# Kernel tuning notes

Hardware: AMD Instinct MI355X
Metric: run time of the kernel (lower is better)

The kernel has to match this reference:

```python
import jax, jax.numpy as jnp
import numpy as np

NUM_GROUPS = 32
NUM_HEAD_CH = 64
EPS = 1e-5


def setup_inputs() -> dict:
    key = jax.random.key(0)
    k1, k2, k3 = jax.random.split(key, 3)
    B, C, H, W = 16, 512, 32, 32
    return {
        "x": jax.random.normal(k1, (B, C, H, W), dtype=jnp.float32),
        "norm_w": jnp.ones((C,), dtype=jnp.float32),
        "norm_b": jnp.zeros((C,), dtype=jnp.float32),
        "qkv_w": jax.random.normal(k2, (3 * C, C), dtype=jnp.float32) * 0.02,
        "qkv_b": jnp.zeros((3 * C,), dtype=jnp.float32),
        "proj_w": jax.random.normal(k3, (C, C), dtype=jnp.float32) * 0.02,
        "proj_b": jnp.zeros((C,), dtype=jnp.float32),
    }


def _group_norm(x, w, b):
    # x: [B, C, T]
    B, C, T = x.shape
    g = x.reshape(B, NUM_GROUPS, C // NUM_GROUPS, T)
    mean = g.mean(axis=(2, 3), keepdims=True)
    var = g.var(axis=(2, 3), keepdims=True)
    g = (g - mean) * jax.lax.rsqrt(var + EPS)
    return g.reshape(B, C, T) * w[None, :, None] + b[None, :, None]


def reference(x, norm_w, norm_b, qkv_w, qkv_b, proj_w, proj_b):
    B, C, Hs, Ws = x.shape
    T = Hs * Ws
    xr = x.reshape(B, C, T)
    xn = _group_norm(xr, norm_w, norm_b)
    # 1x1 conv == matmul over channel dim
    qkv = jnp.einsum('oc,bct->bot', qkv_w, xn) + qkv_b[None, :, None]  # [B, 3C, T]
    q, k, v = jnp.split(qkv, 3, axis=1)
    nH = C // NUM_HEAD_CH
    ch = NUM_HEAD_CH
    q = q.reshape(B * nH, ch, T)
    k = k.reshape(B * nH, ch, T)
    v = v.reshape(B * nH, ch, T)
    scale = 1.0 / np.sqrt(np.sqrt(ch)).astype(np.float32)
    # [BH, T, S] score matrix, softmax in float32 (matches torch .float())
    weight = jnp.einsum('bct,bcs->bts', q * scale, k * scale)
    weight = jax.nn.softmax(weight.astype(jnp.float32), axis=-1).astype(weight.dtype)
    a = jnp.einsum('bts,bcs->bct', weight, v).reshape(B, C, T)
    h = jnp.einsum('oc,bct->bot', proj_w, a) + proj_b[None, :, None]
    return (xr + h).reshape(B, C, Hs, Ws)
```

## Files before the change

### kernel.cpp

```cpp
#include <hip/hip_runtime.h>
#include <hip/hip_bf16.h>


typedef __bf16 bf16x8 __attribute__((ext_vector_type(8)));
typedef __bf16 bf16x4 __attribute__((ext_vector_type(4)));
typedef float f32x4 __attribute__((ext_vector_type(4)));

#define MFMA16(a, b, c) __builtin_amdgcn_mfma_f32_16x16x32_bf16((a), (b), (c), 0, 0, 0)

typedef const __attribute__((address_space(1))) unsigned int* gptr_t;
typedef __attribute__((address_space(3))) unsigned int* lptr_t;

__device__ __forceinline__ void gload16(const void* g, void* l) {
  __builtin_amdgcn_global_load_lds((gptr_t)g, (lptr_t)l, 16, 0, 0);
}

__global__ __launch_bounds__(256) void gn_cvt_kernel(const float* __restrict__ x,
                                                     const float* __restrict__ nw,
                                                     const float* __restrict__ nb,
                                                     __hip_bfloat16* __restrict__ xnt,
                                                     const float* __restrict__ qw,
                                                     __hip_bfloat16* __restrict__ qwb,
                                                     const float* __restrict__ pw,
                                                     __hip_bfloat16* __restrict__ pwb) {
  const int blk = blockIdx.x;
  if (blk >= 512) {
    const int base = (blk - 512) * 256 + threadIdx.x;
#pragma unroll
    for (int t = 0; t < 4; ++t) {
      int i = base + t * 65536;
      const float* src;
      __hip_bfloat16* dst;
      if (i < 196608) { src = qw; dst = qwb; }
      else            { i -= 196608; src = pw; dst = pwb; }
      float4 v = ((const float4*)src)[i];
      union { __hip_bfloat16 h[4]; uint2 u; } pk;
      pk.h[0] = __float2bfloat16(v.x);
      pk.h[1] = __float2bfloat16(v.y);
      pk.h[2] = __float2bfloat16(v.z);
      pk.h[3] = __float2bfloat16(v.w);
      *(uint2*)(dst + (size_t)i * 4) = pk.u;
    }
    return;
  }
  const int bb = blk & 15, g = blk >> 4;
  const int tid = threadIdx.x;
  const float4* xg = (const float4*)(x + ((size_t)bb * 512 + g * 16) * 1024);

  float4 vals[16];
  float s = 0.f, ss = 0.f;
#pragma unroll
  for (int k = 0; k < 16; ++k) {
    float4 v = xg[tid + 256 * k];
    vals[k] = v;
    s += v.x + v.y + v.z + v.w;
    ss += v.x * v.x + v.y * v.y + v.z * v.z + v.w * v.w;
  }
#pragma unroll
  for (int off = 1; off < 64; off <<= 1) {
    s += __shfl_xor(s, off, 64);
    ss += __shfl_xor(ss, off, 64);
  }
  __shared__ float red[8];
  const int wid = tid >> 6, lane = tid & 63;
  if (lane == 0) { red[wid] = s; red[wid + 4] = ss; }
  __syncthreads();
  s = red[0] + red[1] + red[2] + red[3];
  ss = red[4] + red[5] + red[6] + red[7];
  const float mean = s * (1.f / 16384.f);
  const float var = ss * (1.f / 16384.f) - mean * mean;
  const float rstd = rsqrtf(var + 1e-5f);

  float aa[16], cc[16];
#pragma unroll
  for (int k = 0; k < 16; ++k) {
    float w = nw[g * 16 + k];
    float b = nb[g * 16 + k];
    aa[k] = rstd * w;
    cc[k] = b - mean * aa[k];
  }
#pragma unroll
  for (int j = 0; j < 4; ++j) {
    union { __hip_bfloat16 h[16]; uint4 u[2]; } row;
#pragma unroll
    for (int k = 0; k < 16; ++k) {
      float v = ((const float*)&vals[k])[j];
      row.h[k] = __float2bfloat16(v * aa[k] + cc[k]);
    }
    size_t idx = ((size_t)bb * 1024 + 4 * tid + j) * 512 + g * 16;
    *(uint4*)(xnt + idx) = row.u[0];
    *(uint4*)(xnt + idx + 8) = row.u[1];
  }
}

template <int EPI>
__global__ __launch_bounds__(512) void gemm_bt(const __hip_bfloat16* __restrict__ A,
                                               const __hip_bfloat16* __restrict__ Bt,
                                               const float* __restrict__ bias,
                                               __hip_bfloat16* __restrict__ oq,
                                               __hip_bfloat16* __restrict__ ok,
                                               __hip_bfloat16* __restrict__ ov,
                                               const float* __restrict__ xres,
                                               float* __restrict__ of) {
  __shared__ __hip_bfloat16 Alds[128 * 64];
  __shared__ __hip_bfloat16 Blds[256 * 64];
  const int tid = threadIdx.x;
  const int wid = tid >> 6, lane = tid & 63;
  const int g = lane >> 4, tl = lane & 15;
  const int wr = wid >> 2, wc = wid & 3;
  const int NM = (EPI == 0) ? 12 : 4;
  const int id = blockIdx.x;
  const int xcd = id & 7, w = id >> 3;
  const int m0 = (w % NM) * 128;
  const int n0 = (xcd * 8 + w / NM) * 256;

  const int srow8 = lane >> 3;
  const int sselem = ((lane & 7) * 8) ^ (srow8 << 3);
  const int rswz = (tl & 7) << 4;

  f32x4 acc[4][4];
#pragma unroll
  for (int i = 0; i < 4; ++i)
#pragma unroll
    for (int j = 0; j < 4; ++j) acc[i][j] = (f32x4){0.f, 0.f, 0.f, 0.f};

  for (int kt = 0; kt < 8; ++kt) {
    const int k0 = kt * 64;
    __syncthreads();
#pragma unroll
    for (int q = 0; q < 2; ++q) {
      const int r = q * 64 + wid * 8 + srow8;
      gload16(A + (size_t)(m0 + r) * 512 + k0 + sselem,
              (char*)Alds + q * 8192 + wid * 1024);
    }
#pragma unroll
    for (int q = 0; q < 4; ++q) {
      const int r = q * 64 + wid * 8 + srow8;
      gload16(Bt + (size_t)(n0 + r) * 512 + k0 + sselem,
              (char*)Blds + q * 8192 + wid * 1024);
    }
    __syncthreads();
#pragma unroll
    for (int kk = 0; kk < 2; ++kk) {
      bf16x8 af[4], bfr[4];
#pragma unroll
      for (int mi = 0; mi < 4; ++mi) {
        const int row = wr * 64 + mi * 16 + tl;
        af[mi] = *(const bf16x8*)((char*)Alds + row * 128 + ((kk * 64 + g * 16) ^ rswz));
      }
#pragma unroll
      for (int ni = 0; ni < 4; ++ni) {
        const int row = wc * 64 + ni * 16 + tl;
        bfr[ni] = *(const bf16x8*)((char*)Blds + row * 128 + ((kk * 64 + g * 16) ^ rswz));
      }
      __builtin_amdgcn_s_setprio(1);
#pragma unroll
      for (int mi = 0; mi < 4; ++mi)
#pragma unroll
        for (int ni = 0; ni < 4; ++ni)
          acc[mi][ni] = MFMA16(af[mi], bfr[ni], acc[mi][ni]);
      __builtin_amdgcn_s_setprio(0);
    }
  }

  if (EPI == 0) {
    const bool isv = (m0 >= 1024);
    const bool isq = (m0 < 512);
    const float qs = 0.42466090014286f;
#pragma unroll
    for (int mi = 0; mi < 4; ++mi) {
      const int o = m0 + wr * 64 + mi * 16 + g * 4;
      const int och = o & 511, h = och >> 6, cb = och & 63;
#pragma unroll
      for (int ni = 0; ni < 4; ++ni) {
        const int n = n0 + wc * 64 + ni * 16 + tl;
        const int bb2 = n >> 10, t = n & 1023;
        const int bh = bb2 * 8 + h;
        if (!isv) {
          union { __hip_bfloat16 h4[4]; uint2 u; } pk;
#pragma unroll
          for (int r = 0; r < 4; ++r)
            pk.h4[r] = __float2bfloat16((acc[mi][ni][r] + bias[o + r]) * qs);
          __hip_bfloat16* dst = (isq ? oq : ok) + ((size_t)bh * 1024 + t) * 64 + cb;
          *(uint2*)dst = pk.u;
        } else {
#pragma unroll
          for (int r = 0; r < 4; ++r)
            ov[((size_t)bh * 64 + cb + r) * 1024 + t] =
                __float2bfloat16(acc[mi][ni][r] + bias[o + r]);
        }
      }
    }
  } else {
#pragma unroll
    for (int mi = 0; mi < 4; ++mi) {
#pragma unroll
      for (int r = 0; r < 4; ++r) {
        const int o = m0 + wr * 64 + mi * 16 + g * 4 + r;
        const float bv = bias[o];
#pragma unroll
        for (int ni = 0; ni < 4; ++ni) {
          const int n = n0 + wc * 64 + ni * 16 + tl;
          const int bb2 = n >> 10, t = n & 1023;
          const size_t xi = ((size_t)bb2 * 512 + o) * 1024 + t;
          of[xi] = xres[xi] + acc[mi][ni][r] + bv;
        }
      }
    }
  }
}

__global__ __launch_bounds__(512) void attn_kernel(
    const __hip_bfloat16* __restrict__ qt,
    const __hip_bfloat16* __restrict__ kt,
    const __hip_bfloat16* __restrict__ vv,
    __hip_bfloat16* __restrict__ at) {
  const int blk = blockIdx.x;
  const int xcd = blk & 7;
  const int within = blk >> 3;
  const int tile = within & 3;
  const int bhi = xcd * 16 + (within >> 2);
  const int tid = threadIdx.x;
  const int wid = tid >> 6, lane = tid & 63;
  const int g = lane >> 4, tl = lane & 15;
  const int t0 = tile * 256 + wid * 32;

  const char* qh = (const char*)(qt + (size_t)bhi * 65536);
  const char* kh = (const char*)(kt + (size_t)bhi * 65536);
  const char* vh = (const char*)(vv + (size_t)bhi * 65536);

  __shared__ __hip_bfloat16 Klds[3][4096];
  __shared__ __hip_bfloat16 Vlds[3][4096];
  __shared__ __hip_bfloat16 Plds[8][2048];

  const int swz = (tl & 7) << 4;
  char* Pw = (char*)&Plds[wid][0];

  const int srow = lane >> 3;
  const int grow = wid * 8 + srow;
  const int ssw = ((lane & 7) * 16) ^ ((srow & 7) << 4);

  bf16x8 qb[2][2];
#pragma unroll
  for (int qs = 0; qs < 2; ++qs)
#pragma unroll
    for (int h = 0; h < 2; ++h)
      qb[qs][h] = *(const bf16x8*)(qh + (size_t)(t0 + qs * 16 + tl) * 128 + h * 64 + g * 16);

  bf16x8 vones;
#pragma unroll
  for (int i = 0; i < 8; ++i) vones[i] = (__bf16)1.0f;

  f32x4 acc[2][4];
  f32x4 accl[2];
#pragma unroll
  for (int i = 0; i < 2; ++i) {
    accl[i] = (f32x4){0.f, 0.f, 0.f, 0.f};
#pragma unroll
    for (int j = 0; j < 4; ++j) acc[i][j] = (f32x4){0.f, 0.f, 0.f, 0.f};
  }

  gload16(kh + (size_t)grow * 128 + ssw, (char*)&Klds[0][0] + wid * 1024);
  gload16(vh + (size_t)grow * 2048 + ssw, (char*)&Vlds[0][0] + wid * 1024);
  gload16(kh + (size_t)(64 + grow) * 128 + ssw, (char*)&Klds[1][0] + wid * 1024);
  gload16(vh + (size_t)grow * 2048 + 128 + ssw, (char*)&Vlds[1][0] + wid * 1024);
  asm volatile("s_waitcnt vmcnt(2)" ::: "memory");
  __builtin_amdgcn_s_barrier();

  for (int sb = 0; sb < 16; ++sb) {
    {
      const int nt = (sb + 2) & 15;
      const int nbuf = (sb + 2) % 3;
      gload16(kh + (size_t)(nt * 64 + grow) * 128 + ssw,
              (char*)&Klds[nbuf][0] + wid * 1024);
      gload16(vh + (size_t)grow * 2048 + nt * 128 + ssw,
              (char*)&Vlds[nbuf][0] + wid * 1024);
    }
    const int cb = sb % 3;
    const char* Kb = (const char*)&Klds[cb][0];
    const char* Vb = (const char*)&Vlds[cb][0];

    f32x4 sv[4][2];
#pragma unroll
    for (int st = 0; st < 4; ++st) {
      const int krow = (st * 16 + tl) * 128;
      bf16x8 ka0 = *(const bf16x8*)(Kb + krow + ((g * 16) ^ swz));
      bf16x8 ka1 = *(const bf16x8*)(Kb + krow + ((64 + g * 16) ^ swz));
      __builtin_amdgcn_s_setprio(1);
#pragma unroll
      for (int qs = 0; qs < 2; ++qs) {
        f32x4 z = (f32x4){0.f, 0.f, 0.f, 0.f};
        z = MFMA16(ka0, qb[qs][0], z);
        z = MFMA16(ka1, qb[qs][1], z);
        sv[st][qs] = z;
      }
      __builtin_amdgcn_s_setprio(0);
    }

#pragma unroll
    for (int qs = 0; qs < 2; ++qs) {
#pragma unroll
      for (int st = 0; st < 4; ++st) {
        bf16x4 pu;
#pragma unroll
        for (int r = 0; r < 4; ++r) {
          float p = exp2f(sv[st][qs][r]);
          pu[r] = (__bf16)p;
        }
        *(bf16x4*)(Pw + (qs * 16 + tl) * 128 + ((st * 32 + g * 8) ^ swz)) = pu;
      }
    }

    bf16x8 pa[2][2];
#pragma unroll
    for (int ts = 0; ts < 2; ++ts) {
      const int prow = (ts * 16 + tl) * 128;
      pa[ts][0] = *(const bf16x8*)(Pw + prow + ((g * 16) ^ swz));
      pa[ts][1] = *(const bf16x8*)(Pw + prow + ((64 + g * 16) ^ swz));
    }
    __builtin_amdgcn_s_setprio(1);
#pragma unroll
    for (int ts = 0; ts < 2; ++ts) {
      accl[ts] = MFMA16(pa[ts][0], vones, accl[ts]);
      accl[ts] = MFMA16(pa[ts][1], vones, accl[ts]);
    }
    __builtin_amdgcn_s_setprio(0);
#pragma unroll
    for (int ct = 0; ct < 4; ++ct) {
      const int vrow = (ct * 16 + tl) * 128;
      bf16x8 vb0 = *(const bf16x8*)(Vb + vrow + ((g * 16) ^ swz));
      bf16x8 vb1 = *(const bf16x8*)(Vb + vrow + ((64 + g * 16) ^ swz));
      __builtin_amdgcn_s_setprio(1);
#pragma unroll
      for (int ts = 0; ts < 2; ++ts) {
        acc[ts][ct] = MFMA16(pa[ts][0], vb0, acc[ts][ct]);
        acc[ts][ct] = MFMA16(pa[ts][1], vb1, acc[ts][ct]);
      }
      __builtin_amdgcn_s_setprio(0);
    }
    asm volatile("s_waitcnt vmcnt(2)" ::: "memory");
    __builtin_amdgcn_s_barrier();
  }

  const int bb2 = bhi >> 3, hh = bhi & 7;
#pragma unroll
  for (int ts = 0; ts < 2; ++ts) {
#pragma unroll
    for (int r = 0; r < 4; ++r) {
      const float iv = 1.f / accl[ts][r];
      const size_t row = (size_t)bb2 * 1024 + t0 + ts * 16 + g * 4 + r;
#pragma unroll
      for (int ct = 0; ct < 4; ++ct)
        at[row * 512 + hh * 64 + ct * 16 + tl] = __float2bfloat16(acc[ts][ct][r] * iv);
    }
  }
}

extern "C" void kernel_launch(void* const* d_in, const int* in_sizes, int n_in,
                              void* d_out, int out_size, void* d_ws, size_t ws_size,
                              hipStream_t stream) {
  const float* x  = (const float*)d_in[0];
  const float* nw = (const float*)d_in[1];
  const float* nb = (const float*)d_in[2];
  const float* qw = (const float*)d_in[3];
  const float* qb = (const float*)d_in[4];
  const float* pw = (const float*)d_in[5];
  const float* pb = (const float*)d_in[6];
  float* out = (float*)d_out;
  char* ws = (char*)d_ws;

  __hip_bfloat16* xnt = (__hip_bfloat16*)(ws);
  __hip_bfloat16* qtb = (__hip_bfloat16*)(ws + 16777216);
  __hip_bfloat16* ktb = (__hip_bfloat16*)(ws + 33554432);
  __hip_bfloat16* vvb = (__hip_bfloat16*)(ws + 50331648);
  __hip_bfloat16* qwb = (__hip_bfloat16*)(ws + 67108864);
  __hip_bfloat16* pwb = (__hip_bfloat16*)(ws + 68681728);

  gn_cvt_kernel<<<768, 256, 0, stream>>>(x, nw, nb, xnt, qw, qwb, pw, pwb);
  gemm_bt<0><<<768, 512, 0, stream>>>(qwb, xnt, qb, qtb, ktb, vvb,
                                      nullptr, nullptr);
  attn_kernel<<<512, 512, 0, stream>>>(qtb, ktb, vvb, xnt);
  gemm_bt<1><<<256, 512, 0, stream>>>(pwb, xnt, pb, nullptr, nullptr,
                                      nullptr, x, out);
}
```

Before: 136.3 us.

## Double query rows per attention wave and switch to double-buffered K/V

Each wave now handles 64 query rows instead of 32, so each block covers 512 queries and the grid shrinks to 256 blocks. Each K/V tile loaded into LDS is therefore reused across twice as many queries. The triple-buffered prefetch with partial vmcnt waits is replaced by double buffering with full __syncthreads. The cost is more registers per wave and a larger P scratch area, which may reduce occupancy and weaken load/compute overlap.

```diff
diff --git a/kernel.cpp b/kernel.cpp
--- a/kernel.cpp
+++ b/kernel.cpp
@@ -210,7 +210,7 @@
   }
 }
 
-__global__ __launch_bounds__(512) void attn_kernel(
+__global__ __launch_bounds__(512, 2) void attn_kernel(
     const __hip_bfloat16* __restrict__ qt,
     const __hip_bfloat16* __restrict__ kt,
     const __hip_bfloat16* __restrict__ vv,
@@ -218,20 +218,20 @@
   const int blk = blockIdx.x;
   const int xcd = blk & 7;
   const int within = blk >> 3;
-  const int tile = within & 3;
-  const int bhi = xcd * 16 + (within >> 2);
+  const int tile = within & 1;
+  const int bhi = xcd * 16 + (within >> 1);
   const int tid = threadIdx.x;
   const int wid = tid >> 6, lane = tid & 63;
   const int g = lane >> 4, tl = lane & 15;
-  const int t0 = tile * 256 + wid * 32;
+  const int t0 = tile * 512 + wid * 64;
 
   const char* qh = (const char*)(qt + (size_t)bhi * 65536);
   const char* kh = (const char*)(kt + (size_t)bhi * 65536);
   const char* vh = (const char*)(vv + (size_t)bhi * 65536);
 
-  __shared__ __hip_bfloat16 Klds[3][4096];
-  __shared__ __hip_bfloat16 Vlds[3][4096];
-  __shared__ __hip_bfloat16 Plds[8][2048];
+  __shared__ __hip_bfloat16 Klds[2][4096];
+  __shared__ __hip_bfloat16 Vlds[2][4096];
+  __shared__ __hip_bfloat16 Plds[8][4096];
 
   const int swz = (tl & 7) << 4;
   char* Pw = (char*)&Plds[wid][0];
@@ -240,9 +240,9 @@
   const int grow = wid * 8 + srow;
   const int ssw = ((lane & 7) * 16) ^ ((srow & 7) << 4);
 
-  bf16x8 qb[2][2];
-#pragma unroll
-  for (int qs = 0; qs < 2; ++qs)
+  bf16x8 qb[4][2];
+#pragma unroll
+  for (int qs = 0; qs < 4; ++qs)
 #pragma unroll
     for (int h = 0; h < 2; ++h)
       qb[qs][h] = *(const bf16x8*)(qh + (size_t)(t0 + qs * 16 + tl) * 128 + h * 64 + g * 16);
@@ -251,10 +251,10 @@
 #pragma unroll
   for (int i = 0; i < 8; ++i) vones[i] = (__bf16)1.0f;
 
-  f32x4 acc[2][4];
-  f32x4 accl[2];
-#pragma unroll
-  for (int i = 0; i < 2; ++i) {
+  f32x4 acc[4][4];
+  f32x4 accl[4];
+#pragma unroll
+  for (int i = 0; i < 4; ++i) {
     accl[i] = (f32x4){0.f, 0.f, 0.f, 0.f};
 #pragma unroll
     for (int j = 0; j < 4; ++j) acc[i][j] = (f32x4){0.f, 0.f, 0.f, 0.f};
@@ -262,25 +262,21 @@
 
   gload16(kh + (size_t)grow * 128 + ssw, (char*)&Klds[0][0] + wid * 1024);
   gload16(vh + (size_t)grow * 2048 + ssw, (char*)&Vlds[0][0] + wid * 1024);
-  gload16(kh + (size_t)(64 + grow) * 128 + ssw, (char*)&Klds[1][0] + wid * 1024);
-  gload16(vh + (size_t)grow * 2048 + 128 + ssw, (char*)&Vlds[1][0] + wid * 1024);
-  asm volatile("s_waitcnt vmcnt(2)" ::: "memory");
-  __builtin_amdgcn_s_barrier();
-
+  __syncthreads();
+
+  int cur = 0;
   for (int sb = 0; sb < 16; ++sb) {
-    {
-      const int nt = (sb + 2) & 15;
-      const int nbuf = (sb + 2) % 3;
-      gload16(kh + (size_t)(nt * 64 + grow) * 128 + ssw,
-              (char*)&Klds[nbuf][0] + wid * 1024);
-      gload16(vh + (size_t)grow * 2048 + nt * 128 + ssw,
-              (char*)&Vlds[nbuf][0] + wid * 1024);
-    }
-    const int cb = sb % 3;
-    const char* Kb = (const char*)&Klds[cb][0];
-    const char* Vb = (const char*)&Vlds[cb][0];
-
-    f32x4 sv[4][2];
+    if (sb < 15) {
+      const int s0n = (sb + 1) * 64;
+      gload16(kh + (size_t)(s0n + grow) * 128 + ssw,
+              (char*)&Klds[cur ^ 1][0] + wid * 1024);
+      gload16(vh + (size_t)grow * 2048 + s0n * 2 + ssw,
+              (char*)&Vlds[cur ^ 1][0] + wid * 1024);
+    }
+    const char* Kb = (const char*)&Klds[cur][0];
+    const char* Vb = (const char*)&Vlds[cur][0];
+
+    f32x4 sv[4][4];
 #pragma unroll
     for (int st = 0; st < 4; ++st) {
       const int krow = (st * 16 + tl) * 128;
@@ -288,7 +284,7 @@
       bf16x8 ka1 = *(const bf16x8*)(Kb + krow + ((64 + g * 16) ^ swz));
       __builtin_amdgcn_s_setprio(1);
 #pragma unroll
-      for (int qs = 0; qs < 2; ++qs) {
+      for (int qs = 0; qs < 4; ++qs) {
         f32x4 z = (f32x4){0.f, 0.f, 0.f, 0.f};
         z = MFMA16(ka0, qb[qs][0], z);
         z = MFMA16(ka1, qb[qs][1], z);
@@ -298,7 +294,7 @@
     }
 
 #pragma unroll
-    for (int qs = 0; qs < 2; ++qs) {
+    for (int qs = 0; qs < 4; ++qs) {
 #pragma unroll
       for (int st = 0; st < 4; ++st) {
         bf16x4 pu;
@@ -311,18 +307,18 @@
       }
     }
 
-    bf16x8 pa[2][2];
-#pragma unroll
-    for (int ts = 0; ts < 2; ++ts) {
-      const int prow = (ts * 16 + tl) * 128;
-      pa[ts][0] = *(const bf16x8*)(Pw + prow + ((g * 16) ^ swz));
-      pa[ts][1] = *(const bf16x8*)(Pw + prow + ((64 + g * 16) ^ swz));
+    bf16x8 pa[4][2];
+#pragma unroll
+    for (int qs = 0; qs < 4; ++qs) {
+      const int prow = (qs * 16 + tl) * 128;
+      pa[qs][0] = *(const bf16x8*)(Pw + prow + ((g * 16) ^ swz));
+      pa[qs][1] = *(const bf16x8*)(Pw + prow + ((64 + g * 16) ^ swz));
     }
     __builtin_amdgcn_s_setprio(1);
 #pragma unroll
-    for (int ts = 0; ts < 2; ++ts) {
-      accl[ts] = MFMA16(pa[ts][0], vones, accl[ts]);
-      accl[ts] = MFMA16(pa[ts][1], vones, accl[ts]);
+    for (int qs = 0; qs < 4; ++qs) {
+      accl[qs] = MFMA16(pa[qs][0], vones, accl[qs]);
+      accl[qs] = MFMA16(pa[qs][1], vones, accl[qs]);
     }
     __builtin_amdgcn_s_setprio(0);
 #pragma unroll
@@ -332,26 +328,26 @@
       bf16x8 vb1 = *(const bf16x8*)(Vb + vrow + ((64 + g * 16) ^ swz));
       __builtin_amdgcn_s_setprio(1);
 #pragma unroll
-      for (int ts = 0; ts < 2; ++ts) {
-        acc[ts][ct] = MFMA16(pa[ts][0], vb0, acc[ts][ct]);
-        acc[ts][ct] = MFMA16(pa[ts][1], vb1, acc[ts][ct]);
+      for (int qs = 0; qs < 4; ++qs) {
+        acc[qs][ct] = MFMA16(pa[qs][0], vb0, acc[qs][ct]);
+        acc[qs][ct] = MFMA16(pa[qs][1], vb1, acc[qs][ct]);
       }
       __builtin_amdgcn_s_setprio(0);
     }
-    asm volatile("s_waitcnt vmcnt(2)" ::: "memory");
-    __builtin_amdgcn_s_barrier();
+    __syncthreads();
+    cur ^= 1;
   }
 
   const int bb2 = bhi >> 3, hh = bhi & 7;
 #pragma unroll
-  for (int ts = 0; ts < 2; ++ts) {
+  for (int qs = 0; qs < 4; ++qs) {
 #pragma unroll
     for (int r = 0; r < 4; ++r) {
-      const float iv = 1.f / accl[ts][r];
-      const size_t row = (size_t)bb2 * 1024 + t0 + ts * 16 + g * 4 + r;
+      const float iv = 1.f / accl[qs][r];
+      const size_t row = (size_t)bb2 * 1024 + t0 + qs * 16 + g * 4 + r;
 #pragma unroll
       for (int ct = 0; ct < 4; ++ct)
-        at[row * 512 + hh * 64 + ct * 16 + tl] = __float2bfloat16(acc[ts][ct][r] * iv);
+        at[row * 512 + hh * 64 + ct * 16 + tl] = __float2bfloat16(acc[qs][ct][r] * iv);
     }
   }
 }
@@ -379,7 +375,7 @@
   gn_cvt_kernel<<<768, 256, 0, stream>>>(x, nw, nb, xnt, qw, qwb, pw, pwb);
   gemm_bt<0><<<768, 512, 0, stream>>>(qwb, xnt, qb, qtb, ktb, vvb,
                                       nullptr, nullptr);
-  attn_kernel<<<512, 512, 0, stream>>>(qtb, ktb, vvb, xnt);
+  attn_kernel<<<256, 512, 0, stream>>>(qtb, ktb, vvb, xnt);
   gemm_bt<1><<<256, 512, 0, stream>>>(pwb, xnt, pb, nullptr, nullptr,
                                       nullptr, x, out);
 }
```

Result: slower. 140.9 us (+3.4%).

## Transpose softmax probabilities in registers via permlane swaps instead of LDS round-trip

Applied to the files above, without the earlier changes.

The attention kernel no longer writes exp2 probabilities to a per-wave LDS buffer and reads them back as MFMA A-operands. It packs them into bf16 pairs and rearranges them across lanes with v_permlane32/16_swap instructions. The K/V staging also drops from a triple buffer with a prefetch distance of two to a double buffer with __syncthreads, which cuts LDS use and may allow more blocks per CU. In exchange, load/compute overlap shrinks and each barrier now waits for all outstanding loads.

```diff
diff --git a/kernel.cpp b/kernel.cpp
--- a/kernel.cpp
+++ b/kernel.cpp
@@ -13,6 +13,13 @@
 
 __device__ __forceinline__ void gload16(const void* g, void* l) {
   __builtin_amdgcn_global_load_lds((gptr_t)g, (lptr_t)l, 16, 0, 0);
+}
+
+__device__ __forceinline__ unsigned pkbf(float a, float b) {
+  union { __bf16 h[2]; unsigned u; } p;
+  p.h[0] = (__bf16)a;
+  p.h[1] = (__bf16)b;
+  return p.u;
 }
 
 __global__ __launch_bounds__(256) void gn_cvt_kernel(const float* __restrict__ x,
@@ -229,12 +236,10 @@
   const char* kh = (const char*)(kt + (size_t)bhi * 65536);
   const char* vh = (const char*)(vv + (size_t)bhi * 65536);
 
-  __shared__ __hip_bfloat16 Klds[3][4096];
-  __shared__ __hip_bfloat16 Vlds[3][4096];
-  __shared__ __hip_bfloat16 Plds[8][2048];
+  __shared__ __hip_bfloat16 Klds[2][4096];
+  __shared__ __hip_bfloat16 Vlds[2][4096];
 
   const int swz = (tl & 7) << 4;
-  char* Pw = (char*)&Plds[wid][0];
 
   const int srow = lane >> 3;
   const int grow = wid * 8 + srow;
@@ -262,23 +267,19 @@
 
   gload16(kh + (size_t)grow * 128 + ssw, (char*)&Klds[0][0] + wid * 1024);
   gload16(vh + (size_t)grow * 2048 + ssw, (char*)&Vlds[0][0] + wid * 1024);
-  gload16(kh + (size_t)(64 + grow) * 128 + ssw, (char*)&Klds[1][0] + wid * 1024);
-  gload16(vh + (size_t)grow * 2048 + 128 + ssw, (char*)&Vlds[1][0] + wid * 1024);
-  asm volatile("s_waitcnt vmcnt(2)" ::: "memory");
-  __builtin_amdgcn_s_barrier();
-
+  __syncthreads();
+
+  int cur = 0;
   for (int sb = 0; sb < 16; ++sb) {
-    {
-      const int nt = (sb + 2) & 15;
-      const int nbuf = (sb + 2) % 3;
-      gload16(kh + (size_t)(nt * 64 + grow) * 128 + ssw,
-              (char*)&Klds[nbuf][0] + wid * 1024);
-      gload16(vh + (size_t)grow * 2048 + nt * 128 + ssw,
-              (char*)&Vlds[nbuf][0] + wid * 1024);
-    }
-    const int cb = sb % 3;
-    const char* Kb = (const char*)&Klds[cb][0];
-    const char* Vb = (const char*)&Vlds[cb][0];
+    if (sb < 15) {
+      const int s0n = (sb + 1) * 64;
+      gload16(kh + (size_t)(s0n + grow) * 128 + ssw,
+              (char*)&Klds[cur ^ 1][0] + wid * 1024);
+      gload16(vh + (size_t)grow * 2048 + s0n * 2 + ssw,
+              (char*)&Vlds[cur ^ 1][0] + wid * 1024);
+    }
+    const char* Kb = (const char*)&Klds[cur][0];
+    const char* Vb = (const char*)&Vlds[cur][0];
 
     f32x4 sv[4][2];
 #pragma unroll
@@ -297,27 +298,30 @@
       __builtin_amdgcn_s_setprio(0);
     }
 
+    bf16x8 pa[2][2];
 #pragma unroll
     for (int qs = 0; qs < 2; ++qs) {
+      unsigned c[4][2];
 #pragma unroll
       for (int st = 0; st < 4; ++st) {
-        bf16x4 pu;
-#pragma unroll
-        for (int r = 0; r < 4; ++r) {
-          float p = exp2f(sv[st][qs][r]);
-          pu[r] = (__bf16)p;
-        }
-        *(bf16x4*)(Pw + (qs * 16 + tl) * 128 + ((st * 32 + g * 8) ^ swz)) = pu;
-      }
-    }
-
-    bf16x8 pa[2][2];
-#pragma unroll
-    for (int ts = 0; ts < 2; ++ts) {
-      const int prow = (ts * 16 + tl) * 128;
-      pa[ts][0] = *(const bf16x8*)(Pw + prow + ((g * 16) ^ swz));
-      pa[ts][1] = *(const bf16x8*)(Pw + prow + ((64 + g * 16) ^ swz));
-    }
+#pragma unroll
+        for (int h = 0; h < 2; ++h)
+          c[st][h] = pkbf(exp2f(sv[st][qs][2 * h]), exp2f(sv[st][qs][2 * h + 1]));
+      }
+#pragma unroll
+      for (int kk = 0; kk < 2; ++kk) {
+        unsigned x0 = c[2 * kk][0], y0 = c[2 * kk + 1][0];
+        asm("v_permlane32_swap_b32 %0, %1" : "+v"(x0), "+v"(y0));
+        asm("v_permlane16_swap_b32 %0, %1" : "+v"(x0), "+v"(y0));
+        unsigned x1 = c[2 * kk][1], y1 = c[2 * kk + 1][1];
+        asm("v_permlane32_swap_b32 %0, %1" : "+v"(x1), "+v"(y1));
+        asm("v_permlane16_swap_b32 %0, %1" : "+v"(x1), "+v"(y1));
+        union { unsigned u[4]; bf16x8 v; } up;
+        up.u[0] = x0; up.u[1] = x1; up.u[2] = y0; up.u[3] = y1;
+        pa[qs][kk] = up.v;
+      }
+    }
+
     __builtin_amdgcn_s_setprio(1);
 #pragma unroll
     for (int ts = 0; ts < 2; ++ts) {
@@ -338,8 +342,8 @@
       }
       __builtin_amdgcn_s_setprio(0);
     }
-    asm volatile("s_waitcnt vmcnt(2)" ::: "memory");
-    __builtin_amdgcn_s_barrier();
+    __syncthreads();
+    cur ^= 1;
   }
 
   const int bb2 = bhi >> 3, hh = bhi & 7;
```

Result: slower. 141.8 us (+4.1%).

## Software-pipeline attention loop so PV MFMA of previous block overlaps current QK

Applied to the files above, without the earlier changes.

Restructures the attention main loop so each iteration runs the P·V and rowsum MFMAs for the previous key block (using P held in registers) before computing exp for the current block. The aim is to let the exp/VALU work and the MFMA work interleave across stages. K moves to double buffering and V stays in a rotating triple buffer, with an epilogue for the last P·V. The prefetch distance drops from two blocks to one, and a full __syncthreads replaces the explicit vmcnt wait, which may expose more load latency.

```diff
diff --git a/kernel.cpp b/kernel.cpp
--- a/kernel.cpp
+++ b/kernel.cpp
@@ -229,7 +229,7 @@
   const char* kh = (const char*)(kt + (size_t)bhi * 65536);
   const char* vh = (const char*)(vv + (size_t)bhi * 65536);
 
-  __shared__ __hip_bfloat16 Klds[3][4096];
+  __shared__ __hip_bfloat16 Klds[2][4096];
   __shared__ __hip_bfloat16 Vlds[3][4096];
   __shared__ __hip_bfloat16 Plds[8][2048];
 
@@ -253,32 +253,33 @@
 
   f32x4 acc[2][4];
   f32x4 accl[2];
+  bf16x8 pa[2][2];
 #pragma unroll
   for (int i = 0; i < 2; ++i) {
     accl[i] = (f32x4){0.f, 0.f, 0.f, 0.f};
 #pragma unroll
     for (int j = 0; j < 4; ++j) acc[i][j] = (f32x4){0.f, 0.f, 0.f, 0.f};
+#pragma unroll
+    for (int kk = 0; kk < 2; ++kk)
+#pragma unroll
+      for (int e = 0; e < 8; ++e) pa[i][kk][e] = (__bf16)0.0f;
   }
 
   gload16(kh + (size_t)grow * 128 + ssw, (char*)&Klds[0][0] + wid * 1024);
   gload16(vh + (size_t)grow * 2048 + ssw, (char*)&Vlds[0][0] + wid * 1024);
-  gload16(kh + (size_t)(64 + grow) * 128 + ssw, (char*)&Klds[1][0] + wid * 1024);
-  gload16(vh + (size_t)grow * 2048 + 128 + ssw, (char*)&Vlds[1][0] + wid * 1024);
-  asm volatile("s_waitcnt vmcnt(2)" ::: "memory");
-  __builtin_amdgcn_s_barrier();
+  *(uint4*)((char*)&Vlds[2][0] + tid * 16) = (uint4){0, 0, 0, 0};
+  __syncthreads();
 
   for (int sb = 0; sb < 16; ++sb) {
-    {
-      const int nt = (sb + 2) & 15;
-      const int nbuf = (sb + 2) % 3;
-      gload16(kh + (size_t)(nt * 64 + grow) * 128 + ssw,
-              (char*)&Klds[nbuf][0] + wid * 1024);
-      gload16(vh + (size_t)grow * 2048 + nt * 128 + ssw,
-              (char*)&Vlds[nbuf][0] + wid * 1024);
-    }
-    const int cb = sb % 3;
-    const char* Kb = (const char*)&Klds[cb][0];
-    const char* Vb = (const char*)&Vlds[cb][0];
+    if (sb < 15) {
+      const int s0n = (sb + 1) * 64;
+      gload16(kh + (size_t)(s0n + grow) * 128 + ssw,
+              (char*)&Klds[(sb + 1) & 1][0] + wid * 1024);
+      gload16(vh + (size_t)grow * 2048 + s0n * 2 + ssw,
+              (char*)&Vlds[(sb + 1) % 3][0] + wid * 1024);
+    }
+    const char* Kb = (const char*)&Klds[sb & 1][0];
+    const char* Vp = (const char*)&Vlds[(sb + 2) % 3][0];
 
     f32x4 sv[4][2];
 #pragma unroll
@@ -297,6 +298,27 @@
       __builtin_amdgcn_s_setprio(0);
     }
 
+    __builtin_amdgcn_s_setprio(1);
+#pragma unroll
+    for (int ts = 0; ts < 2; ++ts) {
+      accl[ts] = MFMA16(pa[ts][0], vones, accl[ts]);
+      accl[ts] = MFMA16(pa[ts][1], vones, accl[ts]);
+    }
+    __builtin_amdgcn_s_setprio(0);
+#pragma unroll
+    for (int ct = 0; ct < 4; ++ct) {
+      const int vrow = (ct * 16 + tl) * 128;
+      bf16x8 vb0 = *(const bf16x8*)(Vp + vrow + ((g * 16) ^ swz));
+      bf16x8 vb1 = *(const bf16x8*)(Vp + vrow + ((64 + g * 16) ^ swz));
+      __builtin_amdgcn_s_setprio(1);
+#pragma unroll
+      for (int ts = 0; ts < 2; ++ts) {
+        acc[ts][ct] = MFMA16(pa[ts][0], vb0, acc[ts][ct]);
+        acc[ts][ct] = MFMA16(pa[ts][1], vb1, acc[ts][ct]);
+      }
+      __builtin_amdgcn_s_setprio(0);
+    }
+
 #pragma unroll
     for (int qs = 0; qs < 2; ++qs) {
 #pragma unroll
@@ -310,36 +332,35 @@
         *(bf16x4*)(Pw + (qs * 16 + tl) * 128 + ((st * 32 + g * 8) ^ swz)) = pu;
       }
     }
-
-    bf16x8 pa[2][2];
 #pragma unroll
     for (int ts = 0; ts < 2; ++ts) {
       const int prow = (ts * 16 + tl) * 128;
       pa[ts][0] = *(const bf16x8*)(Pw + prow + ((g * 16) ^ swz));
       pa[ts][1] = *(const bf16x8*)(Pw + prow + ((64 + g * 16) ^ swz));
     }
+    __syncthreads();
+  }
+
+  {
+    const char* Vp = (const char*)&Vlds[0][0];
     __builtin_amdgcn_s_setprio(1);
 #pragma unroll
     for (int ts = 0; ts < 2; ++ts) {
       accl[ts] = MFMA16(pa[ts][0], vones, accl[ts]);
       accl[ts] = MFMA16(pa[ts][1], vones, accl[ts]);
     }
-    __builtin_amdgcn_s_setprio(0);
 #pragma unroll
     for (int ct = 0; ct < 4; ++ct) {
       const int vrow = (ct * 16 + tl) * 128;
-      bf16x8 vb0 = *(const bf16x8*)(Vb + vrow + ((g * 16) ^ swz));
-      bf16x8 vb1 = *(const bf16x8*)(Vb + vrow + ((64 + g * 16) ^ swz));
-      __builtin_amdgcn_s_setprio(1);
+      bf16x8 vb0 = *(const bf16x8*)(Vp + vrow + ((g * 16) ^ swz));
+      bf16x8 vb1 = *(const bf16x8*)(Vp + vrow + ((64 + g * 16) ^ swz));
 #pragma unroll
       for (int ts = 0; ts < 2; ++ts) {
         acc[ts][ct] = MFMA16(pa[ts][0], vb0, acc[ts][ct]);
         acc[ts][ct] = MFMA16(pa[ts][1], vb1, acc[ts][ct]);
       }
-      __builtin_amdgcn_s_setprio(0);
-    }
-    asm volatile("s_waitcnt vmcnt(2)" ::: "memory");
-    __builtin_amdgcn_s_barrier();
+    }
+    __builtin_amdgcn_s_setprio(0);
   }
 
   const int bb2 = bhi >> 3, hh = bhi & 7;
```

New measurement: 148.3 us. 1.09x slower.
